# Kernel optimization log

Measured on AMD Instinct MI355X. Metric: run time of the kernel, lower is better.

The kernel has to match this reference:

```python
import jax, jax.numpy as jnp
import numpy as np
from jax import lax

B, C, H, W = 4, 512, 64, 64
DIM = 8              # per-head dim
HEADS = 64           # in_channels // dim
TD = HEADS * DIM     # 512
QKV_CH = 3 * TD      # 1536
PW_GROUPS = 3 * HEADS  # 192
EPS = 1e-5
BN_EPS = 1e-5


def setup_inputs() -> dict:
    key = jax.random.key(0)
    ks = jax.random.split(key, 7)
    s = 0.05
    x = jax.random.normal(ks[0], (B, C, H, W), jnp.float32)
    w_qkv = jax.random.normal(ks[1], (QKV_CH, C), jnp.float32) * s          # 1x1 conv, no bias
    w_dw = jax.random.normal(ks[2], (QKV_CH, 1, 5, 5), jnp.float32) * s     # depthwise 5x5, groups=1536
    w_pw = jax.random.normal(ks[3], (PW_GROUPS, DIM, DIM), jnp.float32) * s  # grouped 1x1, groups=192, 8->8 per group
    w_proj = jax.random.normal(ks[4], (C, 2 * TD), jnp.float32) * s         # 1x1 conv 1024->512
    bn_gamma = 1.0 + 0.1 * jax.random.normal(ks[5], (C,), jnp.float32)
    bn_beta = 0.1 * jax.random.normal(ks[6], (C,), jnp.float32)
    bn_mean = jnp.zeros((C,), jnp.float32)
    bn_var = jnp.ones((C,), jnp.float32)
    return dict(x=x, w_qkv=w_qkv, w_dw=w_dw, w_pw=w_pw, w_proj=w_proj,
                bn_gamma=bn_gamma, bn_beta=bn_beta, bn_mean=bn_mean, bn_var=bn_var)


def reference(x, w_qkv, w_dw, w_pw, w_proj, bn_gamma, bn_beta, bn_mean, bn_var):
    # qkv: 1x1 conv (no norm/act)
    qkv = jnp.einsum('bchw,oc->bohw', x, w_qkv)  # [B,1536,H,W]

    # multi-scale aggregation: depthwise 5x5 then grouped 1x1 (groups=3*heads)
    dw = lax.conv_general_dilated(
        qkv, w_dw, window_strides=(1, 1), padding=[(2, 2), (2, 2)],
        dimension_numbers=('NCHW', 'OIHW', 'NCHW'), feature_group_count=QKV_CH)
    g = dw.reshape(B, PW_GROUPS, DIM, H, W)
    agg = jnp.einsum('bgihw,goi->bgohw', g, w_pw).reshape(B, QKV_CH, H, W)

    # concat scales -> [B, 2*1536, H, W] -> [B, 2*3*heads=... , 3*dim, HW] -> tokens
    ms = jnp.concatenate([qkv, agg], axis=1)
    ms = ms.reshape(B, -1, 3 * DIM, H * W).transpose(0, 1, 3, 2)  # [B, 128, HW, 24]

    q = jax.nn.relu(ms[..., :DIM])
    k = jax.nn.relu(ms[..., DIM:2 * DIM])
    v = ms[..., 2 * DIM:]
    v = jnp.pad(v, ((0, 0), (0, 0), (0, 0), (0, 1)), constant_values=1.0)  # [B,128,HW,9]

    # linear attention core in fp32
    dtype = v.dtype
    q32, k32, v32 = q.astype(jnp.float32), k.astype(jnp.float32), v.astype(jnp.float32)
    kv = jnp.einsum('bhnd,bhne->bhde', k32, v32)   # [B,128,8,9]
    out = jnp.einsum('bhnd,bhde->bhne', q32, kv)   # [B,128,HW,9]
    out = out[..., :-1] / (out[..., -1:] + EPS)
    out = out.astype(dtype)

    out = out.transpose(0, 1, 3, 2).reshape(B, 2 * TD, H, W)  # [B,1024,H,W]

    # proj: 1x1 conv + BatchNorm2d (eval) + no act
    y = jnp.einsum('bchw,oc->bohw', out, w_proj)
    inv = bn_gamma / jnp.sqrt(bn_var + BN_EPS)
    y = y * inv[None, :, None, None] + (bn_beta - bn_mean * inv)[None, :, None, None]
    return y
```

## Files before the change

kernel.cpp:

```cpp
#include <hip/hip_runtime.h>
#include <hip/hip_bf16.h>
#include <cstdint>

#define BB 4
#define C_IN 512
#define HH 64
#define WW 64
#define HWN 4096
#define QKV_CH 1536
#define PW_GROUPS 192
#define NHEADS2 128
#define TD2 1024
#define EPS_F 1e-5f
#define BN_EPS_F 1e-5f

__global__ __launch_bounds__(256) void gemm_f64acc(
    const float* __restrict__ A, const float* __restrict__ Bm,
    float* __restrict__ Cm, int M, int N, int K)
{
    __shared__ float As[8][64];
    __shared__ float Bs[8][128];
    const int bz = blockIdx.z;
    const float* Bp = Bm + (size_t)bz * K * N;
    float*       Cp = Cm + (size_t)bz * M * N;
    const int m0 = blockIdx.y * 64;
    const int n0 = blockIdx.x * 128;
    const int tid = threadIdx.x;
    const int tx = tid & 15;
    const int ty = tid >> 4;

    const int a_row = tid >> 1;
    const int a_col = (tid & 1) << 2;
    const int b_row = tid >> 5;
    const int b_col = (tid & 31) << 2;

    const float* Aptr = A + (size_t)(m0 + a_row) * K + a_col;
    const float* Bptr = Bp + (size_t)b_row * N + n0 + b_col;

    float4 av = make_float4(0.f, 0.f, 0.f, 0.f);
    if (tid < 128) av = *reinterpret_cast<const float4*>(Aptr);
    float4 bv = *reinterpret_cast<const float4*>(Bptr);

    double acc[4][8];
#pragma unroll
    for (int i = 0; i < 4; ++i)
#pragma unroll
        for (int j = 0; j < 8; ++j) acc[i][j] = 0.0;

    for (int k0 = 0; k0 < K; k0 += 8) {
        if (tid < 128) {
            As[a_col + 0][a_row] = av.x;
            As[a_col + 1][a_row] = av.y;
            As[a_col + 2][a_row] = av.z;
            As[a_col + 3][a_row] = av.w;
        }
        *reinterpret_cast<float4*>(&Bs[b_row][b_col]) = bv;
        __syncthreads();
        if (k0 + 8 < K) {
            if (tid < 128) av = *reinterpret_cast<const float4*>(Aptr + k0 + 8);
            bv = *reinterpret_cast<const float4*>(Bptr + (size_t)(k0 + 8) * N);
        }
#pragma unroll
        for (int kk = 0; kk < 8; ++kk) {
            float am[4], bn[8];
            *reinterpret_cast<float4*>(&am[0]) = *reinterpret_cast<const float4*>(&As[kk][ty * 4]);
            *reinterpret_cast<float4*>(&bn[0]) = *reinterpret_cast<const float4*>(&Bs[kk][tx * 8]);
            *reinterpret_cast<float4*>(&bn[4]) = *reinterpret_cast<const float4*>(&Bs[kk][tx * 8 + 4]);
#pragma unroll
            for (int i = 0; i < 4; ++i) {
                const double ad = (double)am[i];
#pragma unroll
                for (int j = 0; j < 8; ++j)
                    acc[i][j] = fma(ad, (double)bn[j], acc[i][j]);
            }
        }
        __syncthreads();
    }

#pragma unroll
    for (int i = 0; i < 4; ++i) {
        float* cp = Cp + (size_t)(m0 + ty * 4 + i) * N + n0 + tx * 8;
        float4 o0, o1;
        o0.x = (float)acc[i][0]; o0.y = (float)acc[i][1];
        o0.z = (float)acc[i][2]; o0.w = (float)acc[i][3];
        o1.x = (float)acc[i][4]; o1.y = (float)acc[i][5];
        o1.z = (float)acc[i][6]; o1.w = (float)acc[i][7];
        *reinterpret_cast<float4*>(cp) = o0;
        *reinterpret_cast<float4*>(cp + 4) = o1;
    }
}

__global__ __launch_bounds__(256) void gemm_f32_epi(
    const float* __restrict__ A,
    const float* __restrict__ B0, const float* __restrict__ B1, int KR0,
    float* __restrict__ Cm, int M, int N, int K,
    const float* __restrict__ g_gamma, const float* __restrict__ g_beta,
    const float* __restrict__ g_mean, const float* __restrict__ g_var)
{
    __shared__ float As[8][128];
    __shared__ float Bs[8][128];
    const int bz = blockIdx.z;
    const float* B0p = B0 + (size_t)bz * KR0 * N;
    const float* B1p = B1 + (size_t)bz * (size_t)(K - KR0) * N - (size_t)KR0 * N;
    float* Cp = Cm + (size_t)bz * M * N;
    const int m0 = blockIdx.y * 128;
    const int n0 = blockIdx.x * 128;
    const int tid = threadIdx.x;
    const int tx = tid & 15;
    const int ty = tid >> 4;

    const int a_row = tid >> 1;
    const int a_col = (tid & 1) << 2;
    const int b_row = tid >> 5;
    const int b_col = (tid & 31) << 2;

    const float* Aptr = A + (size_t)(m0 + a_row) * K + a_col;

    auto loadB = [&](int row) -> float4 {
        const float* base = (row < KR0) ? B0p : B1p;
        return *reinterpret_cast<const float4*>(base + (size_t)row * N + n0 + b_col);
    };

    float4 av = *reinterpret_cast<const float4*>(Aptr);
    float4 bv = loadB(b_row);

    float acc[8][8];
#pragma unroll
    for (int i = 0; i < 8; ++i)
#pragma unroll
        for (int j = 0; j < 8; ++j) acc[i][j] = 0.f;

    for (int k0 = 0; k0 < K; k0 += 8) {
        As[a_col + 0][a_row] = av.x;
        As[a_col + 1][a_row] = av.y;
        As[a_col + 2][a_row] = av.z;
        As[a_col + 3][a_row] = av.w;
        *reinterpret_cast<float4*>(&Bs[b_row][b_col]) = bv;
        __syncthreads();
        if (k0 + 8 < K) {
            av = *reinterpret_cast<const float4*>(Aptr + k0 + 8);
            bv = loadB(k0 + 8 + b_row);
        }
#pragma unroll
        for (int kk = 0; kk < 8; ++kk) {
            float am[8], bn[8];
            *reinterpret_cast<float4*>(&am[0]) = *reinterpret_cast<const float4*>(&As[kk][ty * 8]);
            *reinterpret_cast<float4*>(&am[4]) = *reinterpret_cast<const float4*>(&As[kk][ty * 8 + 4]);
            *reinterpret_cast<float4*>(&bn[0]) = *reinterpret_cast<const float4*>(&Bs[kk][tx * 8]);
            *reinterpret_cast<float4*>(&bn[4]) = *reinterpret_cast<const float4*>(&Bs[kk][tx * 8 + 4]);
#pragma unroll
            for (int i = 0; i < 8; ++i)
#pragma unroll
                for (int j = 0; j < 8; ++j)
                    acc[i][j] = fmaf(am[i], bn[j], acc[i][j]);
        }
        __syncthreads();
    }

#pragma unroll
    for (int i = 0; i < 8; ++i) {
        const int row = m0 + ty * 8 + i;
        const float sc = g_gamma[row] * rsqrtf(g_var[row] + BN_EPS_F);
        const float ad = g_beta[row] - g_mean[row] * sc;
        float* cp = Cp + (size_t)row * N + n0 + tx * 8;
        float4 o0, o1;
        o0.x = acc[i][0] * sc + ad; o0.y = acc[i][1] * sc + ad;
        o0.z = acc[i][2] * sc + ad; o0.w = acc[i][3] * sc + ad;
        o1.x = acc[i][4] * sc + ad; o1.y = acc[i][5] * sc + ad;
        o1.z = acc[i][6] * sc + ad; o1.w = acc[i][7] * sc + ad;
        *reinterpret_cast<float4*>(cp) = o0;
        *reinterpret_cast<float4*>(cp + 4) = o1;
    }
}

__global__ __launch_bounds__(256) void dw_pw(
    const float* __restrict__ qkv, const float* __restrict__ w_dw,
    const float* __restrict__ w_pw, float* __restrict__ agg)
{
    __shared__ float s_in[8][36][36];
    __shared__ float s_wd[200];
    __shared__ float s_wp[64];
    const int g = blockIdx.y;
    const int b = blockIdx.z;
    const int ty0 = (blockIdx.x >> 1) * 32;
    const int tx0 = (blockIdx.x & 1) * 32;
    const int tid = threadIdx.x;

    for (int idx = tid; idx < 8 * 36 * 36; idx += 256) {
        const int i = idx / 1296;
        const int r = idx - i * 1296;
        const int yy = r / 36;
        const int xx = r - yy * 36;
        const int gy = ty0 + yy - 2, gx = tx0 + xx - 2;
        float v = 0.f;
        if (gy >= 0 && gy < HH && gx >= 0 && gx < WW)
            v = qkv[((size_t)b * QKV_CH + g * 8 + i) * HWN + gy * WW + gx];
        s_in[i][yy][xx] = v;
    }
    if (tid < 200) s_wd[tid] = w_dw[(size_t)g * 200 + tid];
    if (tid >= 200 && tid < 264) s_wp[tid - 200] = w_pw[(size_t)g * 64 + tid - 200];
    __syncthreads();

    const int py = tid >> 3;
    const int xq = (tid & 7) << 2;

    double outp[8][4];
#pragma unroll
    for (int o = 0; o < 8; ++o)
#pragma unroll
        for (int p = 0; p < 4; ++p) outp[o][p] = 0.0;

#pragma unroll
    for (int i = 0; i < 8; ++i) {
        double dw4[4] = {0.0, 0.0, 0.0, 0.0};
#pragma unroll
        for (int dy = 0; dy < 5; ++dy) {
            const float* row = &s_in[i][py + dy][xq];
            float rr[8];
            *reinterpret_cast<float4*>(&rr[0]) = *reinterpret_cast<const float4*>(&row[0]);
            *reinterpret_cast<float4*>(&rr[4]) = *reinterpret_cast<const float4*>(&row[4]);
#pragma unroll
            for (int dx = 0; dx < 5; ++dx) {
                const double w = (double)s_wd[i * 25 + dy * 5 + dx];
#pragma unroll
                for (int p = 0; p < 4; ++p)
                    dw4[p] = fma((double)rr[p + dx], w, dw4[p]);
            }
        }
#pragma unroll
        for (int o = 0; o < 8; ++o) {
            const double w = (double)s_wp[o * 8 + i];
#pragma unroll
            for (int p = 0; p < 4; ++p) outp[o][p] = fma(dw4[p], w, outp[o][p]);
        }
    }
#pragma unroll
    for (int o = 0; o < 8; ++o) {
        float4 ov;
        ov.x = (float)outp[o][0]; ov.y = (float)outp[o][1];
        ov.z = (float)outp[o][2]; ov.w = (float)outp[o][3];
        *reinterpret_cast<float4*>(
            &agg[((size_t)b * QKV_CH + g * 8 + o) * HWN + (ty0 + py) * WW + tx0 + xq]) = ov;
    }
}

__global__ __launch_bounds__(256) void kv_reduce(
    const float* __restrict__ qkv, const float* __restrict__ agg,
    float* __restrict__ kv)
{
    const int h = blockIdx.x;
    const int b = blockIdx.y;
    const float* src = (h < 64 ? qkv : agg) + ((size_t)b * QKV_CH + (h & 63) * 24) * HWN;
    const int tid = threadIdx.x;

    float acc[72];
#pragma unroll
    for (int j = 0; j < 72; ++j) acc[j] = 0.f;

    for (int n = tid; n < HWN; n += 256) {
        float kk[8], vv[8];
#pragma unroll
        for (int d = 0; d < 8; ++d) kk[d] = fmaxf(src[(size_t)(8 + d) * HWN + n], 0.f);
#pragma unroll
        for (int e = 0; e < 8; ++e) vv[e] = src[(size_t)(16 + e) * HWN + n];
#pragma unroll
        for (int d = 0; d < 8; ++d) {
#pragma unroll
            for (int e = 0; e < 8; ++e) acc[d * 9 + e] = fmaf(kk[d], vv[e], acc[d * 9 + e]);
            acc[d * 9 + 8] += kk[d];
        }
    }

    __shared__ float red[4][72];
    const int lane = tid & 63, wid = tid >> 6;
#pragma unroll
    for (int j = 0; j < 72; ++j) {
        float v = acc[j];
#pragma unroll
        for (int off = 32; off >= 1; off >>= 1) v += __shfl_xor(v, off);
        if (lane == 0) red[wid][j] = v;
    }
    __syncthreads();
    if (tid < 72) {
        const float s = red[0][tid] + red[1][tid] + red[2][tid] + red[3][tid];
        kv[((size_t)b * NHEADS2 + h) * 72 + tid] = s;
    }
}

__global__ __launch_bounds__(256) void attn_out(
    const float* __restrict__ src_all, const float* __restrict__ kv,
    float* __restrict__ dst, int h_off)
{
    const int hl = blockIdx.x;
    const int b = blockIdx.y;
    const float* src = src_all + ((size_t)b * QKV_CH + hl * 24) * HWN;
    __shared__ float skv[72];
    if (threadIdx.x < 72)
        skv[threadIdx.x] = kv[((size_t)b * NHEADS2 + h_off + hl) * 72 + threadIdx.x];
    __syncthreads();
    float* dstp = dst + ((size_t)b * 512 + hl * 8) * HWN;

    for (int n = threadIdx.x; n < HWN; n += 256) {
        float q[8];
#pragma unroll
        for (int d = 0; d < 8; ++d) q[d] = fmaxf(src[(size_t)d * HWN + n], 0.f);
        float num[9];
#pragma unroll
        for (int e = 0; e < 9; ++e) {
            float s = 0.f;
#pragma unroll
            for (int d = 0; d < 8; ++d) s = fmaf(q[d], skv[d * 9 + e], s);
            num[e] = s;
        }
        const float r = 1.f / (num[8] + EPS_F);
#pragma unroll
        for (int e = 0; e < 8; ++e) dstp[(size_t)e * HWN + n] = num[e] * r;
    }
}

extern "C" void kernel_launch(void* const* d_in, const int* in_sizes, int n_in,
                              void* d_out, int out_size, void* d_ws, size_t ws_size,
                              hipStream_t stream)
{
    const float* x      = (const float*)d_in[0];
    const float* w_qkv  = (const float*)d_in[1];
    const float* w_dw   = (const float*)d_in[2];
    const float* w_pw   = (const float*)d_in[3];
    const float* w_proj = (const float*)d_in[4];
    const float* gamma  = (const float*)d_in[5];
    const float* beta   = (const float*)d_in[6];
    const float* mean   = (const float*)d_in[7];
    const float* var    = (const float*)d_in[8];
    float* out = (float*)d_out;

    float* kv     = (float*)d_ws;
    float* qkv    = kv + (size_t)BB * NHEADS2 * 72;
    float* agg    = qkv + (size_t)BB * NHEADS2 * 0 + (size_t)BB * QKV_CH * HWN + ((size_t)BB * NHEADS2 * 72 - (size_t)BB * NHEADS2 * 72);
    qkv    = kv + (size_t)BB * NHEADS2 * 72;
    agg    = qkv + (size_t)BB * QKV_CH * HWN;
    float* out_tA = agg + (size_t)BB * QKV_CH * HWN;
    float* out_tB = qkv;

    gemm_f64acc<<<dim3(HWN / 128, QKV_CH / 64, BB), 256, 0, stream>>>(
        w_qkv, x, qkv, QKV_CH, HWN, C_IN);

    dw_pw<<<dim3(4, PW_GROUPS, BB), 256, 0, stream>>>(qkv, w_dw, w_pw, agg);

    kv_reduce<<<dim3(NHEADS2, BB), 256, 0, stream>>>(qkv, agg, kv);

    attn_out<<<dim3(64, BB), 256, 0, stream>>>(qkv, kv, out_tA, 0);
    attn_out<<<dim3(64, BB), 256, 0, stream>>>(agg, kv, out_tB, 64);

    gemm_f32_epi<<<dim3(HWN / 128, C_IN / 128, BB), 256, 0, stream>>>(
        w_proj, out_tA, out_tB, 512, out, C_IN, HWN, TD2,
        gamma, beta, mean, var);
}
```

Measured before the change: 931.8 us.

## Split QKV into Q/K/V planes, use fp64 only for Q path, loop per batch

The QKV 1x1 conv is split into three GEMMs via a row remap. Only the Q rows keep fp64 accumulation, while K and V use an fp32 8x8 register-tiled GEMM. The depthwise+pointwise kernel is templated so only the Q part accumulates in double. Execution is restructured into a per-batch loop with separate Q/K/V buffers, which shrinks the workspace but launches many small grids (e.g. 64 or 128 blocks), risking under-occupancy on a large GPU.

```diff
diff --git a/kernel.cpp b/kernel.cpp
--- a/kernel.cpp
+++ b/kernel.cpp
@@ -8,21 +8,23 @@
 #define WW 64
 #define HWN 4096
 #define QKV_CH 1536
-#define PW_GROUPS 192
 #define NHEADS2 128
 #define TD2 1024
 #define EPS_F 1e-5f
 #define BN_EPS_F 1e-5f
 
-__global__ __launch_bounds__(256) void gemm_f64acc(
+__device__ __forceinline__ int amap(int m, int p) {
+    return (m >> 3) * 24 + p * 8 + (m & 7);
+}
+
+__global__ __launch_bounds__(256) void gemm_q_f64(
     const float* __restrict__ A, const float* __restrict__ Bm,
-    float* __restrict__ Cm, int M, int N, int K)
+    float* __restrict__ Cm, int N, int K)
 {
     __shared__ float As[8][64];
     __shared__ float Bs[8][128];
-    const int bz = blockIdx.z;
-    const float* Bp = Bm + (size_t)bz * K * N;
-    float*       Cp = Cm + (size_t)bz * M * N;
+    const float* Bp = Bm;
+    float*       Cp = Cm;
     const int m0 = blockIdx.y * 64;
     const int n0 = blockIdx.x * 128;
     const int tid = threadIdx.x;
@@ -34,7 +36,7 @@
     const int b_row = tid >> 5;
     const int b_col = (tid & 31) << 2;
 
-    const float* Aptr = A + (size_t)(m0 + a_row) * K + a_col;
+    const float* Aptr = A + (size_t)amap(m0 + a_row, 0) * K + a_col;
     const float* Bptr = Bp + (size_t)b_row * N + n0 + b_col;
 
     float4 av = make_float4(0.f, 0.f, 0.f, 0.f);
@@ -90,6 +92,75 @@
     }
 }
 
+__global__ __launch_bounds__(256) void gemm_kv_f32(
+    const float* __restrict__ A, const float* __restrict__ Bm,
+    float* __restrict__ Cm, int N, int K, int p)
+{
+    __shared__ float As[8][128];
+    __shared__ float Bs[8][128];
+    const float* Bp = Bm;
+    float*       Cp = Cm;
+    const int m0 = blockIdx.y * 128;
+    const int n0 = blockIdx.x * 128;
+    const int tid = threadIdx.x;
+    const int tx = tid & 15;
+    const int ty = tid >> 4;
+
+    const int a_row = tid >> 1;
+    const int a_col = (tid & 1) << 2;
+    const int b_row = tid >> 5;
+    const int b_col = (tid & 31) << 2;
+
+    const float* Aptr = A + (size_t)amap(m0 + a_row, p) * K + a_col;
+    const float* Bptr = Bp + (size_t)b_row * N + n0 + b_col;
+
+    float4 av = *reinterpret_cast<const float4*>(Aptr);
+    float4 bv = *reinterpret_cast<const float4*>(Bptr);
+
+    float acc[8][8];
+#pragma unroll
+    for (int i = 0; i < 8; ++i)
+#pragma unroll
+        for (int j = 0; j < 8; ++j) acc[i][j] = 0.f;
+
+    for (int k0 = 0; k0 < K; k0 += 8) {
+        As[a_col + 0][a_row] = av.x;
+        As[a_col + 1][a_row] = av.y;
+        As[a_col + 2][a_row] = av.z;
+        As[a_col + 3][a_row] = av.w;
+        *reinterpret_cast<float4*>(&Bs[b_row][b_col]) = bv;
+        __syncthreads();
+        if (k0 + 8 < K) {
+            av = *reinterpret_cast<const float4*>(Aptr + k0 + 8);
+            bv = *reinterpret_cast<const float4*>(Bptr + (size_t)(k0 + 8) * N);
+        }
+#pragma unroll
+        for (int kk = 0; kk < 8; ++kk) {
+            float am[8], bn[8];
+            *reinterpret_cast<float4*>(&am[0]) = *reinterpret_cast<const float4*>(&As[kk][ty * 8]);
+            *reinterpret_cast<float4*>(&am[4]) = *reinterpret_cast<const float4*>(&As[kk][ty * 8 + 4]);
+            *reinterpret_cast<float4*>(&bn[0]) = *reinterpret_cast<const float4*>(&Bs[kk][tx * 8]);
+            *reinterpret_cast<float4*>(&bn[4]) = *reinterpret_cast<const float4*>(&Bs[kk][tx * 8 + 4]);
+#pragma unroll
+            for (int i = 0; i < 8; ++i)
+#pragma unroll
+                for (int j = 0; j < 8; ++j)
+                    acc[i][j] = fmaf(am[i], bn[j], acc[i][j]);
+        }
+        __syncthreads();
+    }
+
+#pragma unroll
+    for (int i = 0; i < 8; ++i) {
+        float* cp = Cp + (size_t)(m0 + ty * 8 + i) * N + n0 + tx * 8;
+        float4 o0, o1;
+        o0.x = acc[i][0]; o0.y = acc[i][1]; o0.z = acc[i][2]; o0.w = acc[i][3];
+        o1.x = acc[i][4]; o1.y = acc[i][5]; o1.z = acc[i][6]; o1.w = acc[i][7];
+        *reinterpret_cast<float4*>(cp) = o0;
+        *reinterpret_cast<float4*>(cp + 4) = o1;
+    }
+}
+
 __global__ __launch_bounds__(256) void gemm_f32_epi(
     const float* __restrict__ A,
     const float* __restrict__ B0, const float* __restrict__ B1, int KR0,
@@ -99,10 +170,9 @@
 {
     __shared__ float As[8][128];
     __shared__ float Bs[8][128];
-    const int bz = blockIdx.z;
-    const float* B0p = B0 + (size_t)bz * KR0 * N;
-    const float* B1p = B1 + (size_t)bz * (size_t)(K - KR0) * N - (size_t)KR0 * N;
-    float* Cp = Cm + (size_t)bz * M * N;
+    const float* B0p = B0;
+    const float* B1p = B1 - (size_t)KR0 * N;
+    float* Cp = Cm;
     const int m0 = blockIdx.y * 128;
     const int n0 = blockIdx.x * 128;
     const int tid = threadIdx.x;
@@ -173,15 +243,16 @@
     }
 }
 
-__global__ __launch_bounds__(256) void dw_pw(
-    const float* __restrict__ qkv, const float* __restrict__ w_dw,
-    const float* __restrict__ w_pw, float* __restrict__ agg)
+template <typename ACC>
+__global__ __launch_bounds__(256) void dw_pw_part(
+    const float* __restrict__ src, const float* __restrict__ w_dw,
+    const float* __restrict__ w_pw, float* __restrict__ dst, int p)
 {
     __shared__ float s_in[8][36][36];
     __shared__ float s_wd[200];
     __shared__ float s_wp[64];
-    const int g = blockIdx.y;
-    const int b = blockIdx.z;
+    const int h = blockIdx.y;
+    const int g = 3 * h + p;
     const int ty0 = (blockIdx.x >> 1) * 32;
     const int tx0 = (blockIdx.x & 1) * 32;
     const int tid = threadIdx.x;
@@ -194,7 +265,7 @@
         const int gy = ty0 + yy - 2, gx = tx0 + xx - 2;
         float v = 0.f;
         if (gy >= 0 && gy < HH && gx >= 0 && gx < WW)
-            v = qkv[((size_t)b * QKV_CH + g * 8 + i) * HWN + gy * WW + gx];
+            v = src[((size_t)h * 8 + i) * HWN + gy * WW + gx];
         s_in[i][yy][xx] = v;
     }
     if (tid < 200) s_wd[tid] = w_dw[(size_t)g * 200 + tid];
@@ -204,15 +275,15 @@
     const int py = tid >> 3;
     const int xq = (tid & 7) << 2;
 
-    double outp[8][4];
+    ACC outp[8][4];
 #pragma unroll
     for (int o = 0; o < 8; ++o)
 #pragma unroll
-        for (int p = 0; p < 4; ++p) outp[o][p] = 0.0;
+        for (int pp = 0; pp < 4; ++pp) outp[o][pp] = (ACC)0;
 
 #pragma unroll
     for (int i = 0; i < 8; ++i) {
-        double dw4[4] = {0.0, 0.0, 0.0, 0.0};
+        ACC dw4[4] = {(ACC)0, (ACC)0, (ACC)0, (ACC)0};
 #pragma unroll
         for (int dy = 0; dy < 5; ++dy) {
             const float* row = &s_in[i][py + dy][xq];
@@ -221,17 +292,17 @@
             *reinterpret_cast<float4*>(&rr[4]) = *reinterpret_cast<const float4*>(&row[4]);
 #pragma unroll
             for (int dx = 0; dx < 5; ++dx) {
-                const double w = (double)s_wd[i * 25 + dy * 5 + dx];
-#pragma unroll
-                for (int p = 0; p < 4; ++p)
-                    dw4[p] = fma((double)rr[p + dx], w, dw4[p]);
+                const ACC w = (ACC)s_wd[i * 25 + dy * 5 + dx];
+#pragma unroll
+                for (int pp = 0; pp < 4; ++pp)
+                    dw4[pp] += (ACC)rr[pp + dx] * w;
             }
         }
 #pragma unroll
         for (int o = 0; o < 8; ++o) {
-            const double w = (double)s_wp[o * 8 + i];
-#pragma unroll
-            for (int p = 0; p < 4; ++p) outp[o][p] = fma(dw4[p], w, outp[o][p]);
+            const ACC w = (ACC)s_wp[o * 8 + i];
+#pragma unroll
+            for (int pp = 0; pp < 4; ++pp) outp[o][pp] += dw4[pp] * w;
         }
     }
 #pragma unroll
@@ -240,17 +311,19 @@
         ov.x = (float)outp[o][0]; ov.y = (float)outp[o][1];
         ov.z = (float)outp[o][2]; ov.w = (float)outp[o][3];
         *reinterpret_cast<float4*>(
-            &agg[((size_t)b * QKV_CH + g * 8 + o) * HWN + (ty0 + py) * WW + tx0 + xq]) = ov;
+            &dst[((size_t)h * 8 + o) * HWN + (ty0 + py) * WW + tx0 + xq]) = ov;
     }
 }
 
 __global__ __launch_bounds__(256) void kv_reduce(
-    const float* __restrict__ qkv, const float* __restrict__ agg,
+    const float* __restrict__ Ka, const float* __restrict__ Kb,
+    const float* __restrict__ Va, const float* __restrict__ Vb,
     float* __restrict__ kv)
 {
     const int h = blockIdx.x;
-    const int b = blockIdx.y;
-    const float* src = (h < 64 ? qkv : agg) + ((size_t)b * QKV_CH + (h & 63) * 24) * HWN;
+    const size_t off = (size_t)(h & 63) * 8 * HWN;
+    const float* sk = (h < 64 ? Ka : Kb) + off;
+    const float* sv = (h < 64 ? Va : Vb) + off;
     const int tid = threadIdx.x;
 
     float acc[72];
@@ -260,9 +333,9 @@
     for (int n = tid; n < HWN; n += 256) {
         float kk[8], vv[8];
 #pragma unroll
-        for (int d = 0; d < 8; ++d) kk[d] = fmaxf(src[(size_t)(8 + d) * HWN + n], 0.f);
-#pragma unroll
-        for (int e = 0; e < 8; ++e) vv[e] = src[(size_t)(16 + e) * HWN + n];
+        for (int d = 0; d < 8; ++d) kk[d] = fmaxf(sk[(size_t)d * HWN + n], 0.f);
+#pragma unroll
+        for (int e = 0; e < 8; ++e) vv[e] = sv[(size_t)e * HWN + n];
 #pragma unroll
         for (int d = 0; d < 8; ++d) {
 #pragma unroll
@@ -277,28 +350,27 @@
     for (int j = 0; j < 72; ++j) {
         float v = acc[j];
 #pragma unroll
-        for (int off = 32; off >= 1; off >>= 1) v += __shfl_xor(v, off);
+        for (int off2 = 32; off2 >= 1; off2 >>= 1) v += __shfl_xor(v, off2);
         if (lane == 0) red[wid][j] = v;
     }
     __syncthreads();
     if (tid < 72) {
         const float s = red[0][tid] + red[1][tid] + red[2][tid] + red[3][tid];
-        kv[((size_t)b * NHEADS2 + h) * 72 + tid] = s;
+        kv[(size_t)h * 72 + tid] = s;
     }
 }
 
 __global__ __launch_bounds__(256) void attn_out(
-    const float* __restrict__ src_all, const float* __restrict__ kv,
+    const float* __restrict__ Qbuf, const float* __restrict__ kv,
     float* __restrict__ dst, int h_off)
 {
     const int hl = blockIdx.x;
-    const int b = blockIdx.y;
-    const float* src = src_all + ((size_t)b * QKV_CH + hl * 24) * HWN;
+    const float* src = Qbuf + (size_t)hl * 8 * HWN;
     __shared__ float skv[72];
     if (threadIdx.x < 72)
-        skv[threadIdx.x] = kv[((size_t)b * NHEADS2 + h_off + hl) * 72 + threadIdx.x];
+        skv[threadIdx.x] = kv[(size_t)(h_off + hl) * 72 + threadIdx.x];
     __syncthreads();
-    float* dstp = dst + ((size_t)b * 512 + hl * 8) * HWN;
+    float* dstp = dst + (size_t)hl * 8 * HWN;
 
     for (int n = threadIdx.x; n < HWN; n += 256) {
         float q[8];
@@ -333,25 +405,39 @@
     const float* var    = (const float*)d_in[8];
     float* out = (float*)d_out;
 
+    const size_t PSZ = (size_t)512 * HWN;
     float* kv     = (float*)d_ws;
-    float* qkv    = kv + (size_t)BB * NHEADS2 * 72;
-    float* agg    = qkv + (size_t)BB * NHEADS2 * 0 + (size_t)BB * QKV_CH * HWN + ((size_t)BB * NHEADS2 * 72 - (size_t)BB * NHEADS2 * 72);
-    qkv    = kv + (size_t)BB * NHEADS2 * 72;
-    agg    = qkv + (size_t)BB * QKV_CH * HWN;
-    float* out_tA = agg + (size_t)BB * QKV_CH * HWN;
-    float* out_tB = qkv;
-
-    gemm_f64acc<<<dim3(HWN / 128, QKV_CH / 64, BB), 256, 0, stream>>>(
-        w_qkv, x, qkv, QKV_CH, HWN, C_IN);
-
-    dw_pw<<<dim3(4, PW_GROUPS, BB), 256, 0, stream>>>(qkv, w_dw, w_pw, agg);
-
-    kv_reduce<<<dim3(NHEADS2, BB), 256, 0, stream>>>(qkv, agg, kv);
-
-    attn_out<<<dim3(64, BB), 256, 0, stream>>>(qkv, kv, out_tA, 0);
-    attn_out<<<dim3(64, BB), 256, 0, stream>>>(agg, kv, out_tB, 64);
-
-    gemm_f32_epi<<<dim3(HWN / 128, C_IN / 128, BB), 256, 0, stream>>>(
-        w_proj, out_tA, out_tB, 512, out, C_IN, HWN, TD2,
-        gamma, beta, mean, var);
-}
+    float* Qa     = kv + (size_t)NHEADS2 * 72;
+    float* Ka     = Qa + PSZ;
+    float* Va     = Ka + PSZ;
+    float* Qb     = Va + PSZ;
+    float* Kb     = Qb + PSZ;
+    float* Vb     = Kb + PSZ;
+    float* out_tA = Vb + PSZ;
+    float* out_tB = Qa;
+
+    for (int b = 0; b < BB; ++b) {
+        const float* xb   = x + (size_t)b * C_IN * HWN;
+        float*       outb = out + (size_t)b * C_IN * HWN;
+
+        gemm_q_f64<<<dim3(HWN / 128, 8, 1), 256, 0, stream>>>(
+            w_qkv, xb, Qa, HWN, C_IN);
+        gemm_kv_f32<<<dim3(HWN / 128, 4, 1), 256, 0, stream>>>(
+            w_qkv, xb, Ka, HWN, C_IN, 1);
+        gemm_kv_f32<<<dim3(HWN / 128, 4, 1), 256, 0, stream>>>(
+            w_qkv, xb, Va, HWN, C_IN, 2);
+
+        dw_pw_part<double><<<dim3(4, 64, 1), 256, 0, stream>>>(Qa, w_dw, w_pw, Qb, 0);
+        dw_pw_part<float ><<<dim3(4, 64, 1), 256, 0, stream>>>(Ka, w_dw, w_pw, Kb, 1);
+        dw_pw_part<float ><<<dim3(4, 64, 1), 256, 0, stream>>>(Va, w_dw, w_pw, Vb, 2);
+
+        kv_reduce<<<dim3(NHEADS2, 1), 256, 0, stream>>>(Ka, Kb, Va, Vb, kv);
+
+        attn_out<<<dim3(64, 1), 256, 0, stream>>>(Qa, kv, out_tA, 0);
+        attn_out<<<dim3(64, 1), 256, 0, stream>>>(Qb, kv, out_tB, 64);
+
+        gemm_f32_epi<<<dim3(HWN / 128, C_IN / 128, 1), 256, 0, stream>>>(
+            w_proj, out_tA, out_tB, 512, outb, C_IN, HWN, TD2,
+            gamma, beta, mean, var);
+    }
+}
```

Result: slower. 1.759 ms (+88.8%).
